# Kernel optimization log

Measured on AMD Instinct MI355X. Metric: run time of the kernel, lower is better.

## Reference

```python
import jax, jax.numpy as jnp
import numpy as np

N = 50000      # nodes
E = 800000     # edges
IN = 256       # in_dim
H = 8          # heads
C = 32         # out_dim per head (H*C == IN so residual is identity)
NEG_SLOPE = 0.2
LN_EPS = 1e-5


def setup_inputs() -> dict:
    key = jax.random.key(0)
    ks = jax.random.split(key, 8)
    x = jax.random.normal(ks[0], (N, IN), dtype=jnp.float32)
    edge_index = jax.random.randint(ks[1], (2, E), 0, N, dtype=jnp.int64)
    # GATConv params
    W = jax.random.normal(ks[2], (IN, H * C), dtype=jnp.float32) / np.sqrt(IN)
    att_src = jax.random.normal(ks[3], (H, C), dtype=jnp.float32) / np.sqrt(C)
    att_dst = jax.random.normal(ks[4], (H, C), dtype=jnp.float32) / np.sqrt(C)
    bias = jnp.zeros((H * C,), dtype=jnp.float32)
    # LayerNorm params
    ln_scale = jnp.ones((H * C,), dtype=jnp.float32)
    ln_bias = jnp.zeros((H * C,), dtype=jnp.float32)
    return {"x": x, "edge_index": edge_index, "W": W, "att_src": att_src,
            "att_dst": att_dst, "bias": bias, "ln_scale": ln_scale, "ln_bias": ln_bias}


def _gat_block(x, edge_index, W, att_src, att_dst, bias, ln_scale, ln_bias):
    src, dst = edge_index[0], edge_index[1]
    # linear projection -> [N, H, C]
    h = (x @ W).reshape(N, H, C)
    # per-node attention logits [N, H]
    a_src = jnp.einsum('nhc,hc->nh', h, att_src)
    a_dst = jnp.einsum('nhc,hc->nh', h, att_dst)
    # per-edge logits with LeakyReLU [E, H]
    alpha = jax.nn.leaky_relu(a_src[src] + a_dst[dst], NEG_SLOPE)
    # segment softmax over incoming edges of each destination node
    amax = jax.ops.segment_max(alpha, dst, num_segments=N)          # [N, H]
    amax = jnp.where(jnp.isfinite(amax), amax, 0.0)                 # empty segments
    ex = jnp.exp(alpha - amax[dst])                                 # [E, H]
    denom = jax.ops.segment_sum(ex, dst, num_segments=N)           # [N, H]
    attn = ex / (denom[dst] + 1e-16)                                # [E, H]
    # weighted message aggregation -> [N, H, C]
    msg = h[src] * attn[:, :, None]
    out = jax.ops.segment_sum(msg, dst, num_segments=N)
    out = out.reshape(N, H * C) + bias
    # residual (identity since in_dim == heads*out_dim), ELU, LayerNorm
    out = out + x
    out = jax.nn.elu(out)
    mu = jnp.mean(out, axis=-1, keepdims=True)
    var = jnp.var(out, axis=-1, keepdims=True)
    return (out - mu) * jax.lax.rsqrt(var + LN_EPS) * ln_scale + ln_bias


def reference(x, edge_index, W, att_src, att_dst, bias, ln_scale, ln_bias):
    return _gat_block(x, edge_index, W, att_src, att_dst, bias, ln_scale, ln_bias)
```

## Files before the change

### kernel.cpp

```cpp
#include <hip/hip_runtime.h>
#include <hip/hip_bf16.h>
#include <cstdint>

#define NN 50000
#define NE 800000
#define DIM 256
#define NH 8
#define NB 196

typedef short v8s __attribute__((ext_vector_type(8)));
typedef float v4f __attribute__((ext_vector_type(4)));
typedef unsigned short u16x8 __attribute__((ext_vector_type(8)));

__device__ __forceinline__ float b2f(unsigned short u) {
    union { float f; uint32_t i; } c; c.i = ((uint32_t)u) << 16; return c.f;
}
__device__ __forceinline__ unsigned short f2b(float f) {
    union { float f; uint32_t i; } c; c.f = f;
    uint32_t lsb = (c.i >> 16) & 1u;
    return (unsigned short)((c.i + 0x7FFFu + lsb) >> 16);
}

__global__ __launch_bounds__(256) void prep_kernel(
    const float* __restrict__ W, const float* __restrict__ ASRC,
    const float* __restrict__ ADST, unsigned short* __restrict__ Wt) {
    const int t = threadIdx.x;
    if (blockIdx.x < 256) {
        int idx = blockIdx.x * 256 + t;
        int k = idx >> 8, n = idx & 255;
        Wt[n * DIM + k] = f2b(W[k * DIM + n]);
    } else {
        const int k = t;
        #pragma unroll
        for (int h = 0; h < NH; ++h) {
            float ss = 0.f, dd = 0.f;
            #pragma unroll
            for (int c4 = 0; c4 < 8; ++c4) {
                float4 wv = *(const float4*)(W + (size_t)k * DIM + h * 32 + c4 * 4);
                float4 av = *(const float4*)(ASRC + h * 32 + c4 * 4);
                float4 dv = *(const float4*)(ADST + h * 32 + c4 * 4);
                ss += wv.x * av.x + wv.y * av.y + wv.z * av.z + wv.w * av.w;
                dd += wv.x * dv.x + wv.y * dv.y + wv.z * dv.z + wv.w * dv.w;
            }
            Wt[(256 + h) * DIM + k] = f2b(ss);
            Wt[(264 + h) * DIM + k] = f2b(dd);
        }
    }
}

#define LDA3 72
__global__ __launch_bounds__(256) void gemm_kernel(
    const float* __restrict__ X, const unsigned short* __restrict__ Wt,
    const int* __restrict__ e, int* __restrict__ deg,
    unsigned short* __restrict__ H, float* __restrict__ a_srcW,
    float* __restrict__ a_dstW) {
    __shared__ __align__(16) unsigned short As[64 * LDA3];
    __shared__ __align__(16) unsigned short Bs[272 * LDA3];
    const int t = threadIdx.x;
    const int wc = t >> 6, lane = t & 63;
    const int fr = lane & 15, fq = lane >> 4;
    const int m0 = blockIdx.x * 64;

    {
        int probe = e[2 * lane + 1];
        unsigned long long nz = __ballot(probe != 0);
        bool is64 = (nz == 0ull);
        int tg = blockIdx.x * 256 + t;
        #pragma unroll
        for (int j = 0; j < 4; ++j) {
            int i = tg * 4 + j;
            if (i < NE) {
                int d = is64 ? e[2 * (NE + i)] : e[NE + i];
                atomicAdd(&deg[d], 1);
            }
        }
    }

    v4f acc[4][4];
    v4f acc4[4];
    #pragma unroll
    for (int mi = 0; mi < 4; ++mi) {
        acc4[mi] = (v4f){0.f, 0.f, 0.f, 0.f};
        #pragma unroll
        for (int j = 0; j < 4; ++j) acc[mi][j] = (v4f){0.f, 0.f, 0.f, 0.f};
    }

    #pragma unroll
    for (int kt = 0; kt < 256; kt += 64) {
        #pragma unroll
        for (int it = 0; it < 4; ++it) {
            int v = t + it * 256;
            int row = v >> 4;
            int c4 = (v & 15) << 2;
            int gr = m0 + row;
            float4 val = make_float4(0.f, 0.f, 0.f, 0.f);
            if (gr < NN) val = *(const float4*)(X + (size_t)gr * DIM + kt + c4);
            ushort4 o;
            o.x = f2b(val.x); o.y = f2b(val.y); o.z = f2b(val.z); o.w = f2b(val.w);
            *(ushort4*)(As + row * LDA3 + c4) = o;
        }
        #pragma unroll
        for (int it = 0; it < 9; ++it) {
            int v = t + it * 256;
            if (v < 2176) {
                int row = v >> 3;
                int kv = (v & 7) << 3;
                u16x8 val = *(const u16x8*)(Wt + (size_t)row * DIM + kt + kv);
                *(u16x8*)(Bs + row * LDA3 + kv) = val;
            }
        }
        __syncthreads();
        #pragma unroll
        for (int ks = 0; ks < 64; ks += 32) {
            v8s a[4];
            #pragma unroll
            for (int mi = 0; mi < 4; ++mi)
                a[mi] = *(const v8s*)(As + (mi * 16 + fr) * LDA3 + ks + fq * 8);
            #pragma unroll
            for (int j = 0; j < 4; ++j) {
                v8s b = *(const v8s*)(Bs + (wc * 64 + j * 16 + fr) * LDA3 + ks + fq * 8);
                #pragma unroll
                for (int mi = 0; mi < 4; ++mi)
                    acc[mi][j] = __builtin_amdgcn_mfma_f32_16x16x32_bf16(a[mi], b, acc[mi][j], 0, 0, 0);
            }
            if (wc == 0) {
                v8s b4 = *(const v8s*)(Bs + (256 + fr) * LDA3 + ks + fq * 8);
                #pragma unroll
                for (int mi = 0; mi < 4; ++mi)
                    acc4[mi] = __builtin_amdgcn_mfma_f32_16x16x32_bf16(a[mi], b4, acc4[mi], 0, 0, 0);
            }
        }
        __syncthreads();
    }
    #pragma unroll
    for (int mi = 0; mi < 4; ++mi)
        #pragma unroll
        for (int j = 0; j < 4; ++j)
            #pragma unroll
            for (int r = 0; r < 4; ++r) {
                int gr = m0 + mi * 16 + fq * 4 + r;
                int gc = wc * 64 + j * 16 + fr;
                if (gr < NN) H[(size_t)gr * DIM + gc] = f2b(acc[mi][j][r]);
            }
    if (wc == 0) {
        #pragma unroll
        for (int mi = 0; mi < 4; ++mi)
            #pragma unroll
            for (int r = 0; r < 4; ++r) {
                int gr = m0 + mi * 16 + fq * 4 + r;
                if (gr < NN) {
                    if (fr < 8) a_srcW[gr * NH + fr] = acc4[mi][r];
                    else        a_dstW[gr * NH + (fr - 8)] = acc4[mi][r];
                }
            }
    }
}

__global__ __launch_bounds__(256) void scan1_kernel(const int* __restrict__ deg,
                                                    int* __restrict__ row_start,
                                                    int* __restrict__ bsum) {
    const int t = threadIdx.x, b = blockIdx.x;
    const int i = b * 256 + t;
    const int lane = t & 63, wave = t >> 6;
    int v = (i < NN) ? deg[i] : 0;
    int x = v;
    #pragma unroll
    for (int off = 1; off <= 32; off <<= 1) {
        int y = __shfl_up(x, off);
        if (lane >= off) x += y;
    }
    __shared__ int wt[4];
    if (lane == 63) wt[wave] = x;
    __syncthreads();
    int add = 0;
    #pragma unroll
    for (int w2 = 0; w2 < 4; ++w2) if (w2 < wave) add += wt[w2];
    int incl = x + add;
    if (i < NN) row_start[i] = incl - v;
    if (t == 255) bsum[b] = incl;
}

__global__ __launch_bounds__(256) void scan2_kernel(const int* __restrict__ bsum,
                                                    int* __restrict__ boff,
                                                    int* __restrict__ row_start) {
    const int t = threadIdx.x;
    const int lane = t & 63, wave = t >> 6;
    int v = (t < NB) ? bsum[t] : 0;
    int x = v;
    #pragma unroll
    for (int off = 1; off <= 32; off <<= 1) {
        int y = __shfl_up(x, off);
        if (lane >= off) x += y;
    }
    __shared__ int wt[4];
    if (lane == 63) wt[wave] = x;
    __syncthreads();
    int add = 0;
    #pragma unroll
    for (int w2 = 0; w2 < 4; ++w2) if (w2 < wave) add += wt[w2];
    int incl = x + add;
    if (t < NB) boff[t] = incl - v;
    if (t == 255) row_start[NN] = incl;
}

__global__ __launch_bounds__(256) void scan3_kernel(int* __restrict__ row_start,
                                                    const int* __restrict__ boff,
                                                    int* __restrict__ cursor) {
    const int i = blockIdx.x * 256 + threadIdx.x;
    if (i < NN) {
        int r = row_start[i] + boff[blockIdx.x];
        row_start[i] = r;
        cursor[i] = r;
    }
}

__global__ __launch_bounds__(256) void fill_kernel(
    const int* __restrict__ e, const float* __restrict__ a_src,
    const float* __restrict__ a_dst, int* __restrict__ cursor,
    int* __restrict__ csr_src, unsigned short* __restrict__ wcsr16) {
    const int i = blockIdx.x * 256 + threadIdx.x;
    const int lane = threadIdx.x & 63;
    int probe = e[2 * lane + 1];
    unsigned long long nz = __ballot(probe != 0);
    bool is64 = (nz == 0ull);
    int s, d;
    if (is64) { s = e[2 * i]; d = e[2 * (NE + i)]; }
    else      { s = e[i];     d = e[NE + i]; }
    int pos = atomicAdd(&cursor[d], 1);
    csr_src[pos] = s;
    float4 as0 = *(const float4*)(a_src + (size_t)s * NH);
    float4 as1 = *(const float4*)(a_src + (size_t)s * NH + 4);
    float4 ad0 = *(const float4*)(a_dst + (size_t)d * NH);
    float4 ad1 = *(const float4*)(a_dst + (size_t)d * NH + 4);
    const float* asp0 = (const float*)&as0; const float* asp1 = (const float*)&as1;
    const float* adp0 = (const float*)&ad0; const float* adp1 = (const float*)&ad1;
    u16x8 wv;
    #pragma unroll
    for (int h = 0; h < 4; ++h) {
        float lg = asp0[h] + adp0[h];
        lg = lg > 0.f ? lg : 0.2f * lg;
        wv[h] = f2b(__expf(lg));
        float lg2 = asp1[h] + adp1[h];
        lg2 = lg2 > 0.f ? lg2 : 0.2f * lg2;
        wv[4 + h] = f2b(__expf(lg2));
    }
    *(u16x8*)(wcsr16 + (size_t)pos * NH) = wv;
}

__global__ __launch_bounds__(256) void agg_kernel(
    const unsigned short* __restrict__ H, const int* __restrict__ row_start,
    const int* __restrict__ csr_src, const unsigned short* __restrict__ wcsr16,
    const float* __restrict__ X, const float* __restrict__ BIAS,
    const float* __restrict__ LNS, const float* __restrict__ LNB,
    float* __restrict__ OUT) {
    const int wave = threadIdx.x >> 6, lane = threadIdx.x & 63;
    const int d = blockIdx.x * 4 + wave;
    if (d >= NN) return;
    const int base = row_start[d];
    const int degree = row_start[d + 1] - base;
    const int slot = lane >> 5;
    const int q = lane & 31;
    const int headq = q >> 2;

    float4 x0 = *(const float4*)(X + (size_t)d * DIM + q * 8);
    float4 x1 = *(const float4*)(X + (size_t)d * DIM + q * 8 + 4);
    float4 b0 = *(const float4*)(BIAS + q * 8);
    float4 b1 = *(const float4*)(BIAS + q * 8 + 4);
    float4 sc0 = *(const float4*)(LNS + q * 8);
    float4 sc1 = *(const float4*)(LNS + q * 8 + 4);
    float4 lb0 = *(const float4*)(LNB + q * 8);
    float4 lb1 = *(const float4*)(LNB + q * 8 + 4);

    float acc[8];
    #pragma unroll
    for (int j = 0; j < 8; ++j) acc[j] = 0.f;
    float sumw = 0.f;

    for (int c0 = 0; c0 < degree; c0 += 16) {
        const int e0 = c0 + slot * 8;
        const int rem = degree - e0;
        const size_t eb = (size_t)base + e0;
        int s[8]; float w[8];
        #pragma unroll
        for (int k = 0; k < 8; ++k) { s[k] = 0; w[k] = 0.f; }
        #pragma unroll
        for (int k = 0; k < 8; ++k)
            if (rem > k) {
                s[k] = csr_src[eb + k];
                w[k] = b2f(wcsr16[(eb + k) * NH + headq]);
            }
        u16x8 hv[8];
        #pragma unroll
        for (int k = 0; k < 8; ++k)
            hv[k] = *(const u16x8*)(H + (size_t)s[k] * DIM + q * 8);
        #pragma unroll
        for (int k = 0; k < 8; ++k) {
            sumw += w[k];
            #pragma unroll
            for (int j = 0; j < 8; ++j) acc[j] += w[k] * b2f(hv[k][j]);
        }
    }

    float sum_ex = sumw + __shfl_xor(sumw, 32);
    #pragma unroll
    for (int j = 0; j < 8; ++j) acc[j] += __shfl_xor(acc[j], 32);

    const float inv = 1.0f / (sum_ex + 1e-16f);

    const float* xp0 = (const float*)&x0; const float* xp1 = (const float*)&x1;
    const float* bp0 = (const float*)&b0; const float* bp1 = (const float*)&b1;
    float v[8];
    float s1v = 0.f, s2v = 0.f;
    #pragma unroll
    for (int j = 0; j < 8; ++j) {
        float xv = (j < 4) ? xp0[j] : xp1[j - 4];
        float bv = (j < 4) ? bp0[j] : bp1[j - 4];
        float t = acc[j] * inv + bv + xv;
        t = t > 0.f ? t : expm1f(t);
        v[j] = t;
        s1v += t;
        s2v += t * t;
    }
    #pragma unroll
    for (int off = 16; off >= 1; off >>= 1) {
        s1v += __shfl_xor(s1v, off);
        s2v += __shfl_xor(s2v, off);
    }
    const float mean = s1v * (1.0f / 256.0f);
    float var = s2v * (1.0f / 256.0f) - mean * mean;
    var = fmaxf(var, 0.f);
    const float rstd = rsqrtf(var + 1e-5f);

    if (slot == 0) {
        const float* scp0 = (const float*)&sc0; const float* scp1 = (const float*)&sc1;
        const float* lbp0 = (const float*)&lb0; const float* lbp1 = (const float*)&lb1;
        float4 o0, o1;
        float* op0 = (float*)&o0; float* op1 = (float*)&o1;
        #pragma unroll
        for (int j = 0; j < 4; ++j) {
            op0[j] = (v[j] - mean) * rstd * scp0[j] + lbp0[j];
            op1[j] = (v[j + 4] - mean) * rstd * scp1[j] + lbp1[j];
        }
        *(float4*)(OUT + (size_t)d * DIM + q * 8) = o0;
        *(float4*)(OUT + (size_t)d * DIM + q * 8 + 4) = o1;
    }
}

extern "C" void kernel_launch(void* const* d_in, const int* in_sizes, int n_in,
                              void* d_out, int out_size, void* d_ws, size_t ws_size,
                              hipStream_t stream) {
    const float* X    = (const float*)d_in[0];
    const int*   EIDX = (const int*)d_in[1];
    const float* W    = (const float*)d_in[2];
    const float* ASRC = (const float*)d_in[3];
    const float* ADST = (const float*)d_in[4];
    const float* BIAS = (const float*)d_in[5];
    const float* LNS  = (const float*)d_in[6];
    const float* LNB  = (const float*)d_in[7];
    float* OUT = (float*)d_out;

    char* ws = (char*)d_ws;
    unsigned short* H   = (unsigned short*)(ws);
    unsigned short* Wt  = (unsigned short*)(ws + 25600000);
    float* a_srcW       = (float*)(ws + 25739264);
    float* a_dstW       = (float*)(ws + 27339264);
    int*   deg          = (int*)(ws + 28939264);
    int*   row_start    = (int*)(ws + 29139264);
    int*   cursor       = (int*)(ws + 29339280);
    int*   csr_src      = (int*)(ws + 29539280);
    unsigned short* wcsr16 = (unsigned short*)(ws + 32739280);
    int*   bsum         = (int*)(ws + 45539280);
    int*   boff         = (int*)(ws + 45540064);

    hipMemsetAsync(deg, 0, NN * sizeof(int), stream);

    dim3 blk(256);
    prep_kernel<<<dim3(257), blk, 0, stream>>>(W, ASRC, ADST, Wt);
    gemm_kernel<<<dim3(782), blk, 0, stream>>>(X, Wt, EIDX, deg, H, a_srcW, a_dstW);
    scan1_kernel<<<dim3(NB), blk, 0, stream>>>(deg, row_start, bsum);
    scan2_kernel<<<dim3(1), blk, 0, stream>>>(bsum, boff, row_start);
    scan3_kernel<<<dim3(NB), blk, 0, stream>>>(row_start, boff, cursor);
    fill_kernel<<<dim3(NE / 256), blk, 0, stream>>>(EIDX, a_srcW, a_dstW, cursor, csr_src, wcsr16);
    agg_kernel<<<dim3((NN + 3) / 4), blk, 0, stream>>>(
        H, row_start, csr_src, wcsr16, X, BIAS, LNS, LNB, OUT);
}
```

Measured before the change: 320.6 us.

## Replace three-pass scan with single-pass decoupled lookback scan; store fp32 edge weights

Merges the three scan kernels into one decoupled-lookback prefix scan that uses a ticket counter for block ordering and flag-tagged partial sums, so two kernel launches and a round trip through global memory go away. Edge attention weights are now stored as fp32 instead of bf16, which doubles the bytes written in fill and read in agg but drops the bf16 conversions and improves precision. Address arithmetic is switched from size_t to int, which may save some 64-bit index math. The single memset now also clears the ticket and lookback flags.

```diff
diff --git a/kernel.cpp b/kernel.cpp
--- a/kernel.cpp
+++ b/kernel.cpp
@@ -156,10 +156,16 @@
     }
 }
 
-__global__ __launch_bounds__(256) void scan1_kernel(const int* __restrict__ deg,
-                                                    int* __restrict__ row_start,
-                                                    int* __restrict__ bsum) {
-    const int t = threadIdx.x, b = blockIdx.x;
+__global__ __launch_bounds__(256) void scanlb_kernel(
+    const int* __restrict__ deg, int* __restrict__ ticket, int* __restrict__ pay,
+    int* __restrict__ row_start, int* __restrict__ cursor) {
+    __shared__ int sbid;
+    __shared__ int wt[4];
+    __shared__ int sexcl;
+    const int t = threadIdx.x;
+    if (t == 0) sbid = atomicAdd(ticket, 1);
+    __syncthreads();
+    const int b = sbid;
     const int i = b * 256 + t;
     const int lane = t & 63, wave = t >> 6;
     int v = (i < NN) ? deg[i] : 0;
@@ -169,55 +175,41 @@
         int y = __shfl_up(x, off);
         if (lane >= off) x += y;
     }
-    __shared__ int wt[4];
     if (lane == 63) wt[wave] = x;
     __syncthreads();
     int add = 0;
     #pragma unroll
     for (int w2 = 0; w2 < 4; ++w2) if (w2 < wave) add += wt[w2];
-    int incl = x + add;
-    if (i < NN) row_start[i] = incl - v;
-    if (t == 255) bsum[b] = incl;
-}
-
-__global__ __launch_bounds__(256) void scan2_kernel(const int* __restrict__ bsum,
-                                                    int* __restrict__ boff,
-                                                    int* __restrict__ row_start) {
-    const int t = threadIdx.x;
-    const int lane = t & 63, wave = t >> 6;
-    int v = (t < NB) ? bsum[t] : 0;
-    int x = v;
-    #pragma unroll
-    for (int off = 1; off <= 32; off <<= 1) {
-        int y = __shfl_up(x, off);
-        if (lane >= off) x += y;
-    }
-    __shared__ int wt[4];
-    if (lane == 63) wt[wave] = x;
+    const int incl = x + add;
+    const int total = wt[0] + wt[1] + wt[2] + wt[3];
+    if (t == 0) {
+        if (b > 0) atomicExch(&pay[b], (total << 2) | 1);
+        int excl = 0;
+        int p = b - 1;
+        while (p >= 0) {
+            int pv;
+            do { pv = atomicAdd(&pay[p], 0); } while ((pv & 3) == 0);
+            excl += (pv >> 2);
+            if ((pv & 3) == 2) break;
+            --p;
+        }
+        atomicExch(&pay[b], ((excl + total) << 2) | 2);
+        sexcl = excl;
+    }
     __syncthreads();
-    int add = 0;
-    #pragma unroll
-    for (int w2 = 0; w2 < 4; ++w2) if (w2 < wave) add += wt[w2];
-    int incl = x + add;
-    if (t < NB) boff[t] = incl - v;
-    if (t == 255) row_start[NN] = incl;
-}
-
-__global__ __launch_bounds__(256) void scan3_kernel(int* __restrict__ row_start,
-                                                    const int* __restrict__ boff,
-                                                    int* __restrict__ cursor) {
-    const int i = blockIdx.x * 256 + threadIdx.x;
+    const int excl = sexcl;
     if (i < NN) {
-        int r = row_start[i] + boff[blockIdx.x];
+        int r = excl + incl - v;
         row_start[i] = r;
         cursor[i] = r;
     }
+    if (b == NB - 1 && t == 255) row_start[NN] = excl + total;
 }
 
 __global__ __launch_bounds__(256) void fill_kernel(
     const int* __restrict__ e, const float* __restrict__ a_src,
     const float* __restrict__ a_dst, int* __restrict__ cursor,
-    int* __restrict__ csr_src, unsigned short* __restrict__ wcsr16) {
+    int* __restrict__ csr_src, float* __restrict__ wcsr) {
     const int i = blockIdx.x * 256 + threadIdx.x;
     const int lane = threadIdx.x & 63;
     int probe = e[2 * lane + 1];
@@ -228,28 +220,30 @@
     else      { s = e[i];     d = e[NE + i]; }
     int pos = atomicAdd(&cursor[d], 1);
     csr_src[pos] = s;
-    float4 as0 = *(const float4*)(a_src + (size_t)s * NH);
-    float4 as1 = *(const float4*)(a_src + (size_t)s * NH + 4);
-    float4 ad0 = *(const float4*)(a_dst + (size_t)d * NH);
-    float4 ad1 = *(const float4*)(a_dst + (size_t)d * NH + 4);
+    float4 as0 = *(const float4*)(a_src + s * NH);
+    float4 as1 = *(const float4*)(a_src + s * NH + 4);
+    float4 ad0 = *(const float4*)(a_dst + d * NH);
+    float4 ad1 = *(const float4*)(a_dst + d * NH + 4);
     const float* asp0 = (const float*)&as0; const float* asp1 = (const float*)&as1;
     const float* adp0 = (const float*)&ad0; const float* adp1 = (const float*)&ad1;
-    u16x8 wv;
+    float4 w0, w1;
+    float* wp0 = (float*)&w0; float* wp1 = (float*)&w1;
     #pragma unroll
     for (int h = 0; h < 4; ++h) {
         float lg = asp0[h] + adp0[h];
         lg = lg > 0.f ? lg : 0.2f * lg;
-        wv[h] = f2b(__expf(lg));
+        wp0[h] = __expf(lg);
         float lg2 = asp1[h] + adp1[h];
         lg2 = lg2 > 0.f ? lg2 : 0.2f * lg2;
-        wv[4 + h] = f2b(__expf(lg2));
-    }
-    *(u16x8*)(wcsr16 + (size_t)pos * NH) = wv;
+        wp1[h] = __expf(lg2);
+    }
+    *(float4*)(wcsr + pos * NH) = w0;
+    *(float4*)(wcsr + pos * NH + 4) = w1;
 }
 
 __global__ __launch_bounds__(256) void agg_kernel(
     const unsigned short* __restrict__ H, const int* __restrict__ row_start,
-    const int* __restrict__ csr_src, const unsigned short* __restrict__ wcsr16,
+    const int* __restrict__ csr_src, const float* __restrict__ wcsr,
     const float* __restrict__ X, const float* __restrict__ BIAS,
     const float* __restrict__ LNS, const float* __restrict__ LNB,
     float* __restrict__ OUT) {
@@ -261,15 +255,16 @@
     const int slot = lane >> 5;
     const int q = lane & 31;
     const int headq = q >> 2;
-
-    float4 x0 = *(const float4*)(X + (size_t)d * DIM + q * 8);
-    float4 x1 = *(const float4*)(X + (size_t)d * DIM + q * 8 + 4);
-    float4 b0 = *(const float4*)(BIAS + q * 8);
-    float4 b1 = *(const float4*)(BIAS + q * 8 + 4);
-    float4 sc0 = *(const float4*)(LNS + q * 8);
-    float4 sc1 = *(const float4*)(LNS + q * 8 + 4);
-    float4 lb0 = *(const float4*)(LNB + q * 8);
-    float4 lb1 = *(const float4*)(LNB + q * 8 + 4);
+    const int ch0 = q * 8;
+
+    float4 x0 = *(const float4*)(X + d * DIM + ch0);
+    float4 x1 = *(const float4*)(X + d * DIM + ch0 + 4);
+    float4 b0 = *(const float4*)(BIAS + ch0);
+    float4 b1 = *(const float4*)(BIAS + ch0 + 4);
+    float4 sc0 = *(const float4*)(LNS + ch0);
+    float4 sc1 = *(const float4*)(LNS + ch0 + 4);
+    float4 lb0 = *(const float4*)(LNB + ch0);
+    float4 lb1 = *(const float4*)(LNB + ch0 + 4);
 
     float acc[8];
     #pragma unroll
@@ -279,7 +274,7 @@
     for (int c0 = 0; c0 < degree; c0 += 16) {
         const int e0 = c0 + slot * 8;
         const int rem = degree - e0;
-        const size_t eb = (size_t)base + e0;
+        const int eb = base + e0;
         int s[8]; float w[8];
         #pragma unroll
         for (int k = 0; k < 8; ++k) { s[k] = 0; w[k] = 0.f; }
@@ -287,12 +282,12 @@
         for (int k = 0; k < 8; ++k)
             if (rem > k) {
                 s[k] = csr_src[eb + k];
-                w[k] = b2f(wcsr16[(eb + k) * NH + headq]);
+                w[k] = wcsr[(eb + k) * NH + headq];
             }
         u16x8 hv[8];
         #pragma unroll
         for (int k = 0; k < 8; ++k)
-            hv[k] = *(const u16x8*)(H + (size_t)s[k] * DIM + q * 8);
+            hv[k] = *(const u16x8*)(H + s[k] * DIM + ch0);
         #pragma unroll
         for (int k = 0; k < 8; ++k) {
             sumw += w[k];
@@ -341,8 +336,8 @@
             op0[j] = (v[j] - mean) * rstd * scp0[j] + lbp0[j];
             op1[j] = (v[j + 4] - mean) * rstd * scp1[j] + lbp1[j];
         }
-        *(float4*)(OUT + (size_t)d * DIM + q * 8) = o0;
-        *(float4*)(OUT + (size_t)d * DIM + q * 8 + 4) = o1;
+        *(float4*)(OUT + d * DIM + ch0) = o0;
+        *(float4*)(OUT + d * DIM + ch0 + 4) = o1;
     }
 }
 
@@ -365,22 +360,20 @@
     float* a_srcW       = (float*)(ws + 25739264);
     float* a_dstW       = (float*)(ws + 27339264);
     int*   deg          = (int*)(ws + 28939264);
-    int*   row_start    = (int*)(ws + 29139264);
-    int*   cursor       = (int*)(ws + 29339280);
-    int*   csr_src      = (int*)(ws + 29539280);
-    unsigned short* wcsr16 = (unsigned short*)(ws + 32739280);
-    int*   bsum         = (int*)(ws + 45539280);
-    int*   boff         = (int*)(ws + 45540064);
-
-    hipMemsetAsync(deg, 0, NN * sizeof(int), stream);
+    int*   ticket       = (int*)(ws + 29139264);
+    int*   pay          = (int*)(ws + 29139268);
+    int*   row_start    = (int*)(ws + 29140064);
+    int*   cursor       = (int*)(ws + 29340080);
+    int*   csr_src      = (int*)(ws + 29540080);
+    float* wcsr         = (float*)(ws + 32740096);
+
+    hipMemsetAsync(deg, 0, 200788, stream);
 
     dim3 blk(256);
     prep_kernel<<<dim3(257), blk, 0, stream>>>(W, ASRC, ADST, Wt);
     gemm_kernel<<<dim3(782), blk, 0, stream>>>(X, Wt, EIDX, deg, H, a_srcW, a_dstW);
-    scan1_kernel<<<dim3(NB), blk, 0, stream>>>(deg, row_start, bsum);
-    scan2_kernel<<<dim3(1), blk, 0, stream>>>(bsum, boff, row_start);
-    scan3_kernel<<<dim3(NB), blk, 0, stream>>>(row_start, boff, cursor);
-    fill_kernel<<<dim3(NE / 256), blk, 0, stream>>>(EIDX, a_srcW, a_dstW, cursor, csr_src, wcsr16);
+    scanlb_kernel<<<dim3(NB), blk, 0, stream>>>(deg, ticket, pay, row_start, cursor);
+    fill_kernel<<<dim3(NE / 256), blk, 0, stream>>>(EIDX, a_srcW, a_dstW, cursor, csr_src, wcsr);
     agg_kernel<<<dim3((NN + 3) / 4), blk, 0, stream>>>(
-        H, row_start, csr_src, wcsr16, X, BIAS, LNS, LNB, OUT);
-}
+        H, row_start, csr_src, wcsr, X, BIAS, LNS, LNB, OUT);
+}
```

Measured after the change: 314.7 us. No clear change (-1.8%).
